# Kernel tuning notes

Hardware: AMD Instinct MI355X
Metric: run time of the kernel (lower is better)

## Reference

```python
import jax, jax.numpy as jnp
import numpy as np

B, S, D = 4, 2048, 1024
H = 16
DH = D // H  # 64
THETA = 10000.0


def setup_inputs() -> dict:
    key = jax.random.key(0)
    ks = jax.random.split(key, 7)
    scale = 1.0 / np.sqrt(D)
    return {
        "Q": jax.random.normal(ks[0], (B, S, D), dtype=jnp.float32),
        "K": jax.random.normal(ks[1], (B, S, D), dtype=jnp.float32),
        "V": jax.random.normal(ks[2], (B, S, D), dtype=jnp.float32),
        "Wq": jax.random.normal(ks[3], (D, D), dtype=jnp.float32) * scale,
        "Wk": jax.random.normal(ks[4], (D, D), dtype=jnp.float32) * scale,
        "Wv": jax.random.normal(ks[5], (D, D), dtype=jnp.float32) * scale,
        "Wo": jax.random.normal(ks[6], (D, D), dtype=jnp.float32) * scale,
    }


def _rope_tables(seq_len, d_head, theta, dtype):
    inv_freq = 1.0 / theta ** (jnp.arange(0, d_head, 2, dtype=jnp.float32) / d_head)
    ang = jnp.arange(seq_len, dtype=jnp.float32)[:, None] * inv_freq[None, :]  # [S, DH/2]
    return jnp.sin(ang).astype(dtype), jnp.cos(ang).astype(dtype)


def _apply_rope(x, sin, cos):
    # x: [B, H, S, DH]; sin/cos: [S, DH/2] broadcast over B,H
    x1 = x[..., 0::2]
    x2 = x[..., 1::2]
    x1r = x1 * cos - x2 * sin
    x2r = x1 * sin + x2 * cos
    return jnp.stack([x1r, x2r], axis=-1).reshape(x.shape)


def reference(Q, K, V, Wq, Wk, Wv, Wo):
    seq_len = Q.shape[-2]
    q = Q @ Wq.T
    k = K @ Wk.T
    v = V @ Wv.T

    def split(x):  # [B, S, D] -> [B, H, S, DH]
        return x.reshape(x.shape[0], seq_len, H, DH).transpose(0, 2, 1, 3)

    qh, kh, vh = split(q), split(k), split(v)

    sin, cos = _rope_tables(seq_len, DH, THETA, qh.dtype)
    qh = _apply_rope(qh, sin, cos)
    kh = _apply_rope(kh, sin, cos)

    # attention in fp32 (matches original cast)
    qf = qh.astype(jnp.float32)
    kf = kh.astype(jnp.float32)
    vf = vh.astype(jnp.float32)
    scale = 1.0 / np.sqrt(DH)
    scores = jnp.einsum('bhqd,bhkd->bhqk', qf, kf) * scale
    causal = jnp.tril(jnp.ones((seq_len, seq_len), dtype=bool))
    scores = jnp.where(causal, scores, -jnp.inf)
    attn = jax.nn.softmax(scores, axis=-1)
    out_h = jnp.einsum('bhqk,bhkd->bhqd', attn, vf).astype(Q.dtype)

    out = out_h.transpose(0, 2, 1, 3).reshape(Q.shape[0], seq_len, D)
    return out @ Wo.T
```

## Files before the change

kernel.cpp:

```cpp
#include <hip/hip_runtime.h>
#include <hip/hip_bf16.h>
#include <cmath>

#define B_ 4
#define S_ 2048
#define D_ 1024
#define H_ 16
#define DH_ 64

typedef __bf16 bf16_t;
typedef __bf16 bf16x8 __attribute__((ext_vector_type(8)));
typedef __bf16 bf16x4 __attribute__((ext_vector_type(4)));
typedef float f32x4 __attribute__((ext_vector_type(4)));

static __device__ __forceinline__ f32x4 mfma16(bf16x8 a, bf16x8 b, f32x4 c) {
    return __builtin_amdgcn_mfma_f32_16x16x32_bf16(a, b, c, 0, 0, 0);
}

static __device__ __forceinline__ float fast_exp2(float x) {
#if __has_builtin(__builtin_amdgcn_exp2f)
    return __builtin_amdgcn_exp2f(x);
#else
    float r; asm("v_exp_f32 %0, %1" : "=v"(r) : "v"(x)); return r;
#endif
}

static __device__ __forceinline__ void glds16(const void* g, void* l) {
    __builtin_amdgcn_global_load_lds(
        (const __attribute__((address_space(1))) unsigned int*)g,
        (__attribute__((address_space(3))) unsigned int*)l, 16, 0, 0);
}

__global__ __launch_bounds__(256)
void prep_kernel(const float* __restrict__ Wq, const float* __restrict__ Wk,
                 const float* __restrict__ Wv, const float* __restrict__ Wo,
                 bf16_t* __restrict__ Wb, float2* __restrict__ tab)
{
    int bid = blockIdx.x;
    if (bid < 256) {
        int idx = bid * 256 + threadIdx.x;
        int s = idx >> 5, i = idx & 31;
        float inv = powf(10000.f, -(2.f * i) / 64.f);
        float ang = (float)s * inv;
        tab[idx] = make_float2(sinf(ang), cosf(ang));
    } else {
        int i = (bid - 256) * 256 + threadIdx.x;
        int t = i >> 17, j = i & 131071;
        const float* src = (t == 0) ? Wq : (t == 1) ? Wk : (t == 2) ? Wv : Wo;
        const float4* s = (const float4*)(src + (size_t)j * 8);
        float4 a = s[0], b = s[1];
        bf16x8 v = { (__bf16)a.x, (__bf16)a.y, (__bf16)a.z, (__bf16)a.w,
                     (__bf16)b.x, (__bf16)b.y, (__bf16)b.z, (__bf16)b.w };
        *(bf16x8*)(Wb + (size_t)i * 8) = v;
    }
}

template<int EPI>
__global__ __launch_bounds__(256)
void proj_kernel(const float* __restrict__ X, const bf16_t* __restrict__ W,
                 bf16_t* __restrict__ dst, const float2* __restrict__ tab)
{
    __shared__ bf16x8 lA[128 * 8];
    __shared__ bf16x8 lB[128 * 8];
    const int tid = threadIdx.x;
    const int gm0 = blockIdx.x * 128;
    const int gn0 = blockIdx.y * 128;
    const int wid = tid >> 6, lane = tid & 63;
    const int lr = lane & 15, lh = lane >> 4;
    const int wm = (wid >> 1) * 64, wn = (wid & 1) * 64;

    int arow[4], aslot[4];
    const float* abase[4];
    #pragma unroll
    for (int i = 0; i < 4; ++i) {
        int slot = i * 256 + tid;
        int row = slot >> 3, s = slot & 7, c = s ^ (row & 7);
        arow[i] = row; aslot[i] = s;
        abase[i] = X + (size_t)(gm0 + row) * D_ + c * 8;
    }
    float4 av0[4], av1[4];
    #pragma unroll
    for (int i = 0; i < 4; ++i) {
        av0[i] = *(const float4*)(abase[i]);
        av1[i] = *(const float4*)(abase[i] + 4);
    }

    f32x4 acc[4][4] = {};

    #pragma unroll 1
    for (int kt = 0; kt < D_ / 64; ++kt) {
        __syncthreads();
        #pragma unroll
        for (int i = 0; i < 4; ++i) {
            int base = wid * 64 + i * 256;
            int slot = base + lane;
            int row = slot >> 3, s = slot & 7, c = s ^ (row & 7);
            glds16(W + (size_t)(gn0 + row) * D_ + kt * 64 + c * 8, &lB[base]);
        }
        #pragma unroll
        for (int i = 0; i < 4; ++i) {
            lA[arow[i] * 8 + aslot[i]] = bf16x8{
                (__bf16)av0[i].x, (__bf16)av0[i].y, (__bf16)av0[i].z, (__bf16)av0[i].w,
                (__bf16)av1[i].x, (__bf16)av1[i].y, (__bf16)av1[i].z, (__bf16)av1[i].w };
        }
        __syncthreads();
        if (kt + 1 < D_ / 64) {
            #pragma unroll
            for (int i = 0; i < 4; ++i) {
                av0[i] = *(const float4*)(abase[i] + (kt + 1) * 64);
                av1[i] = *(const float4*)(abase[i] + (kt + 1) * 64 + 4);
            }
        }
        #pragma unroll
        for (int ks = 0; ks < 2; ++ks) {
            bf16x8 af[4], bfr[4];
            int kh8 = ks * 4 + lh;
            #pragma unroll
            for (int mi = 0; mi < 4; ++mi) { int r = wm + mi * 16 + lr; af[mi]  = lA[r * 8 + (kh8 ^ (r & 7))]; }
            #pragma unroll
            for (int ni = 0; ni < 4; ++ni) { int r = wn + ni * 16 + lr; bfr[ni] = lB[r * 8 + (kh8 ^ (r & 7))]; }
            #pragma unroll
            for (int mi = 0; mi < 4; ++mi)
                #pragma unroll
                for (int ni = 0; ni < 4; ++ni)
                    acc[mi][ni] = mfma16(af[mi], bfr[ni], acc[mi][ni]);
        }
    }

    #pragma unroll
    for (int mi = 0; mi < 4; ++mi) {
        #pragma unroll
        for (int j = 0; j < 4; ++j) {
            int m = gm0 + wm + mi * 16 + lh * 4 + j;
            int b = m >> 11, s = m & (S_ - 1);
            #pragma unroll
            for (int ni = 0; ni < 4; ++ni) {
                int n = gn0 + wn + ni * 16 + lr;
                int h = n >> 6, dh = n & 63;
                float x = acc[mi][ni][j];
                if (EPI == 0) {
                    float p = __shfl_xor(x, 1);
                    float2 sc = tab[s * 32 + (dh >> 1)];
                    float r = (dh & 1) ? (p * sc.x + x * sc.y)
                                       : (x * sc.y - p * sc.x);
                    dst[(((size_t)b * H_ + h) * S_ + s) * DH_ + dh] = (bf16_t)r;
                } else {
                    dst[(((size_t)b * H_ + h) * DH_ + dh) * S_ + s] = (bf16_t)x;
                }
            }
        }
    }
}

__global__ __launch_bounds__(256, 6)
void attn_kernel(const bf16_t* __restrict__ qh, const bf16_t* __restrict__ kh,
                 const bf16_t* __restrict__ vT, bf16_t* __restrict__ O)
{
    __shared__ bf16x8 lK[64 * 8];
    __shared__ bf16x8 lV[64 * 8];
    __shared__ bf16x8 lP8[4][128];
    const int tid = threadIdx.x, wid = tid >> 6, lane = tid & 63;
    const int lr = lane & 15, lh = lane >> 4;
    const int bh = blockIdx.x & 63;
    const int t  = 31 - (blockIdx.x >> 6);
    const bf16_t* Qp = qh + (size_t)bh * S_ * DH_;
    const bf16_t* Kp = kh + (size_t)bh * S_ * DH_;
    const bf16_t* Vp = vT + (size_t)bh * DH_ * S_;
    char* lP = (char*)lP8[wid];
    const int b = bh >> 4, h = bh & 15;
    const float QSCALE = 0.125f * 1.44269504f;
    const int wq = t * 64 + wid * 16;

    bf16x8 qf[2];
    #pragma unroll
    for (int ks = 0; ks < 2; ++ks) {
        bf16x8 q8 = *(const bf16x8*)(Qp + (size_t)(wq + lr) * DH_ + ks * 32 + lh * 8);
        #pragma unroll
        for (int e = 0; e < 8; ++e) q8[e] = (__bf16)((float)q8[e] * QSCALE);
        qf[ks] = q8;
    }

    f32x4 accO[4] = {};
    float mrun = -1e30f, lrun = 0.f;
    const int nkt = t + 1;

    #pragma unroll 1
    for (int kt = 0; kt < nkt; ++kt) {
        __syncthreads();
        #pragma unroll
        for (int i = 0; i < 2; ++i) {
            int base = i * 256 + (wid << 6);
            int slot = base + lane;
            int row = slot >> 3, s = slot & 7, c = s ^ (row & 7);
            glds16(Kp + (size_t)(kt * 64 + row) * DH_ + c * 8, &lK[base]);
            glds16(Vp + (size_t)row * S_ + kt * 64 + c * 8, &lV[base]);
        }
        __syncthreads();

        f32x4 sc[4] = {};
        __builtin_amdgcn_s_setprio(1);
        #pragma unroll
        for (int ks = 0; ks < 2; ++ks) {
            int kh8 = ks * 4 + lh;
            #pragma unroll
            for (int kvi = 0; kvi < 4; ++kvi) {
                int r = kvi * 16 + lr;
                bf16x8 kf = lK[r * 8 + (kh8 ^ (r & 7))];
                sc[kvi] = mfma16(kf, qf[ks], sc[kvi]);
            }
        }
        __builtin_amdgcn_s_setprio(0);

        const int kvb = kt * 64 + 4 * lh;
        const int qg = wq + lr;
        float pv[16];
        if (kt == t) {
            #pragma unroll
            for (int kvi = 0; kvi < 4; ++kvi)
                #pragma unroll
                for (int j = 0; j < 4; ++j) {
                    float x = sc[kvi][j];
                    if ((kvb + kvi * 16 + j) > qg) x = -1e30f;
                    pv[kvi * 4 + j] = x;
                }
        } else {
            #pragma unroll
            for (int kvi = 0; kvi < 4; ++kvi)
                #pragma unroll
                for (int j = 0; j < 4; ++j) pv[kvi * 4 + j] = sc[kvi][j];
        }

        float t0 = fmaxf(fmaxf(pv[0],  pv[1]),  pv[2]);
        float t1 = fmaxf(fmaxf(pv[3],  pv[4]),  pv[5]);
        float t2 = fmaxf(fmaxf(pv[6],  pv[7]),  pv[8]);
        float t3 = fmaxf(fmaxf(pv[9],  pv[10]), pv[11]);
        float t4 = fmaxf(fmaxf(pv[12], pv[13]), pv[14]);
        float u0 = fmaxf(fmaxf(t0, t1), t2);
        float u1 = fmaxf(fmaxf(t3, t4), pv[15]);
        float mxp = fmaxf(u0, u1);

        float mnew = mrun;
        bool skip = __all(mxp <= mrun + 8.0f);
        if (!skip) {
            float mx = fmaxf(mxp, __shfl_xor(mxp, 16));
            mx = fmaxf(mx, __shfl_xor(mx, 32));
            mnew = fmaxf(mrun, mx);
            float rs = fast_exp2(mrun - mnew);
            mrun = mnew;
            lrun *= rs;
            #pragma unroll
            for (int j = 0; j < 4; ++j) {
                float rj = __shfl(rs, 4 * lh + j);
                #pragma unroll
                for (int ni = 0; ni < 4; ++ni) accO[ni][j] *= rj;
            }
        }
        #pragma unroll
        for (int i = 0; i < 16; ++i) pv[i] = fast_exp2(pv[i] - mnew);
        float s8[8], s4v[4];
        #pragma unroll
        for (int i = 0; i < 8; ++i) s8[i] = pv[i] + pv[i + 8];
        #pragma unroll
        for (int i = 0; i < 4; ++i) s4v[i] = s8[i] + s8[i + 4];
        lrun += (s4v[0] + s4v[1]) + (s4v[2] + s4v[3]);

        #pragma unroll
        for (int kvi = 0; kvi < 4; ++kvi) {
            bf16x4 hv = { (__bf16)pv[kvi * 4 + 0], (__bf16)pv[kvi * 4 + 1],
                          (__bf16)pv[kvi * 4 + 2], (__bf16)pv[kvi * 4 + 3] };
            int slot = 2 * kvi + (lh >> 1);
            *(bf16x4*)(lP + lr * 128 + ((slot ^ (lr & 7)) * 16) + (lh & 1) * 8) = hv;
        }

        __builtin_amdgcn_s_setprio(1);
        #pragma unroll
        for (int ks = 0; ks < 2; ++ks) {
            int kh8 = ks * 4 + lh;
            int slot = 4 * ks + lh;
            bf16x8 pf = *(const bf16x8*)(lP + lr * 128 + ((slot ^ (lr & 7)) * 16));
            #pragma unroll
            for (int ni = 0; ni < 4; ++ni) {
                int r = ni * 16 + lr;
                bf16x8 vf = lV[r * 8 + (kh8 ^ (r & 7))];
                accO[ni] = mfma16(pf, vf, accO[ni]);
            }
        }
        __builtin_amdgcn_s_setprio(0);
    }

    lrun += __shfl_xor(lrun, 16);
    lrun += __shfl_xor(lrun, 32);

    #pragma unroll
    for (int j = 0; j < 4; ++j) {
        int s = wq + 4 * lh + j;
        float inv = 1.f / __shfl(lrun, 4 * lh + j);
        #pragma unroll
        for (int ni = 0; ni < 4; ++ni) {
            int dh = ni * 16 + lr;
            O[((size_t)(b * S_ + s)) * D_ + h * DH_ + dh] = (bf16_t)(accO[ni][j] * inv);
        }
    }
}

__global__ __launch_bounds__(256)
void out_kernel(const bf16_t* __restrict__ A, const bf16_t* __restrict__ W,
                float* __restrict__ out)
{
    __shared__ bf16x8 lA[128 * 8];
    __shared__ bf16x8 lB[128 * 8];
    const int tid = threadIdx.x;
    const int gm0 = blockIdx.x * 128;
    const int gn0 = blockIdx.y * 128;
    const int wid = tid >> 6, lane = tid & 63;
    const int lr = lane & 15, lh = lane >> 4;
    const int wm = (wid >> 1) * 64, wn = (wid & 1) * 64;

    f32x4 acc[4][4] = {};

    for (int kt = 0; kt < D_ / 64; ++kt) {
        const int k0 = kt * 64;
        __syncthreads();
        #pragma unroll
        for (int i = 0; i < 4; ++i) {
            int base = wid * 64 + i * 256;
            int slot = base + lane;
            int row = slot >> 3, s = slot & 7, c = s ^ (row & 7);
            glds16(A + (size_t)(gm0 + row) * D_ + k0 + c * 8, &lA[base]);
            glds16(W + (size_t)(gn0 + row) * D_ + k0 + c * 8, &lB[base]);
        }
        __syncthreads();
        #pragma unroll
        for (int ks = 0; ks < 2; ++ks) {
            bf16x8 af[4], bfr[4];
            int kh = ks * 4 + lh;
            #pragma unroll
            for (int mi = 0; mi < 4; ++mi) { int r = wm + mi * 16 + lr; af[mi]  = lA[r * 8 + (kh ^ (r & 7))]; }
            #pragma unroll
            for (int ni = 0; ni < 4; ++ni) { int r = wn + ni * 16 + lr; bfr[ni] = lB[r * 8 + (kh ^ (r & 7))]; }
            #pragma unroll
            for (int mi = 0; mi < 4; ++mi)
                #pragma unroll
                for (int ni = 0; ni < 4; ++ni)
                    acc[mi][ni] = mfma16(af[mi], bfr[ni], acc[mi][ni]);
        }
    }

    #pragma unroll
    for (int mi = 0; mi < 4; ++mi)
        #pragma unroll
        for (int j = 0; j < 4; ++j) {
            int m = gm0 + wm + mi * 16 + lh * 4 + j;
            #pragma unroll
            for (int ni = 0; ni < 4; ++ni) {
                int n = gn0 + wn + ni * 16 + lr;
                out[(size_t)m * D_ + n] = acc[mi][ni][j];
            }
        }
}

extern "C" void kernel_launch(void* const* d_in, const int* in_sizes, int n_in,
                              void* d_out, int out_size, void* d_ws, size_t ws_size,
                              hipStream_t stream)
{
    const float* Q  = (const float*)d_in[0];
    const float* K  = (const float*)d_in[1];
    const float* V  = (const float*)d_in[2];
    const float* Wq = (const float*)d_in[3];
    const float* Wk = (const float*)d_in[4];
    const float* Wv = (const float*)d_in[5];
    const float* Wo = (const float*)d_in[6];
    float* out = (float*)d_out;

    char* ws = (char*)d_ws;
    const size_t MB = 1024 * 1024;
    bf16_t* qh  = (bf16_t*)(ws);
    bf16_t* khb = (bf16_t*)(ws + 16 * MB);
    bf16_t* vT  = (bf16_t*)(ws + 32 * MB);
    bf16_t* Ob  = (bf16_t*)(ws + 48 * MB);
    bf16_t* Wb  = (bf16_t*)(ws + 64 * MB);
    float2* tab = (float2*)(ws + 72 * MB);

    prep_kernel<<<2304, 256, 0, stream>>>(Wq, Wk, Wv, Wo, Wb, tab);

    dim3 g(64, 8);
    proj_kernel<0><<<g, 256, 0, stream>>>(Q, Wb + 0 * 1048576, qh, tab);
    proj_kernel<0><<<g, 256, 0, stream>>>(K, Wb + 1 * 1048576, khb, tab);
    proj_kernel<1><<<g, 256, 0, stream>>>(V, Wb + 2 * 1048576, vT, tab);

    attn_kernel<<<2048, 256, 0, stream>>>(qh, khb, vT, Ob);

    out_kernel<<<dim3(64, 8), 256, 0, stream>>>(Ob, Wb + 3 * 1048576, out);
}
```

Measured before the change: 180.2 us.

## Double-buffer LDS tiles in projection and output GEMMs to overlap loads

Both the QKV projection GEMM and the output GEMM now use two LDS buffers per operand. The next K-tile is prefetched (glds16 for W/A, register-staged fp32 converted to bf16 for X) while MFMAs run on the current tile, and only one barrier is needed per iteration instead of two. The aim is to hide global-to-LDS latency behind compute. In exchange, LDS use per block doubles, which may lower occupancy. Correctness also depends on the async glds16 writes finishing before the barrier.

```diff
diff --git a/kernel.cpp b/kernel.cpp
--- a/kernel.cpp
+++ b/kernel.cpp
@@ -60,8 +60,8 @@
 void proj_kernel(const float* __restrict__ X, const bf16_t* __restrict__ W,
                  bf16_t* __restrict__ dst, const float2* __restrict__ tab)
 {
-    __shared__ bf16x8 lA[128 * 8];
-    __shared__ bf16x8 lB[128 * 8];
+    __shared__ bf16x8 lA[2][128 * 8];
+    __shared__ bf16x8 lB[2][128 * 8];
     const int tid = threadIdx.x;
     const int gm0 = blockIdx.x * 128;
     const int gn0 = blockIdx.y * 128;
@@ -78,33 +78,42 @@
         arow[i] = row; aslot[i] = s;
         abase[i] = X + (size_t)(gm0 + row) * D_ + c * 8;
     }
+    const bf16_t* bsrc[4]; int bbase[4];
+    #pragma unroll
+    for (int i = 0; i < 4; ++i) {
+        int base = wid * 64 + i * 256;
+        int slot = base + lane;
+        int row = slot >> 3, s = slot & 7, c = s ^ (row & 7);
+        bbase[i] = base;
+        bsrc[i] = W + (size_t)(gn0 + row) * D_ + c * 8;
+    }
+
     float4 av0[4], av1[4];
     #pragma unroll
     for (int i = 0; i < 4; ++i) {
         av0[i] = *(const float4*)(abase[i]);
         av1[i] = *(const float4*)(abase[i] + 4);
     }
+    #pragma unroll
+    for (int i = 0; i < 4; ++i) glds16(bsrc[i], &lB[0][bbase[i]]);
+    #pragma unroll
+    for (int i = 0; i < 4; ++i) {
+        lA[0][arow[i] * 8 + aslot[i]] = bf16x8{
+            (__bf16)av0[i].x, (__bf16)av0[i].y, (__bf16)av0[i].z, (__bf16)av0[i].w,
+            (__bf16)av1[i].x, (__bf16)av1[i].y, (__bf16)av1[i].z, (__bf16)av1[i].w };
+    }
+    __syncthreads();
 
     f32x4 acc[4][4] = {};
+    int cur = 0;
 
     #pragma unroll 1
     for (int kt = 0; kt < D_ / 64; ++kt) {
-        __syncthreads();
-        #pragma unroll
-        for (int i = 0; i < 4; ++i) {
-            int base = wid * 64 + i * 256;
-            int slot = base + lane;
-            int row = slot >> 3, s = slot & 7, c = s ^ (row & 7);
-            glds16(W + (size_t)(gn0 + row) * D_ + kt * 64 + c * 8, &lB[base]);
-        }
-        #pragma unroll
-        for (int i = 0; i < 4; ++i) {
-            lA[arow[i] * 8 + aslot[i]] = bf16x8{
-                (__bf16)av0[i].x, (__bf16)av0[i].y, (__bf16)av0[i].z, (__bf16)av0[i].w,
-                (__bf16)av1[i].x, (__bf16)av1[i].y, (__bf16)av1[i].z, (__bf16)av1[i].w };
-        }
-        __syncthreads();
+        const int nxt = cur ^ 1;
         if (kt + 1 < D_ / 64) {
+            #pragma unroll
+            for (int i = 0; i < 4; ++i)
+                glds16(bsrc[i] + (kt + 1) * 64, &lB[nxt][bbase[i]]);
             #pragma unroll
             for (int i = 0; i < 4; ++i) {
                 av0[i] = *(const float4*)(abase[i] + (kt + 1) * 64);
@@ -116,15 +125,25 @@
             bf16x8 af[4], bfr[4];
             int kh8 = ks * 4 + lh;
             #pragma unroll
-            for (int mi = 0; mi < 4; ++mi) { int r = wm + mi * 16 + lr; af[mi]  = lA[r * 8 + (kh8 ^ (r & 7))]; }
-            #pragma unroll
-            for (int ni = 0; ni < 4; ++ni) { int r = wn + ni * 16 + lr; bfr[ni] = lB[r * 8 + (kh8 ^ (r & 7))]; }
+            for (int mi = 0; mi < 4; ++mi) { int r = wm + mi * 16 + lr; af[mi]  = lA[cur][r * 8 + (kh8 ^ (r & 7))]; }
+            #pragma unroll
+            for (int ni = 0; ni < 4; ++ni) { int r = wn + ni * 16 + lr; bfr[ni] = lB[cur][r * 8 + (kh8 ^ (r & 7))]; }
             #pragma unroll
             for (int mi = 0; mi < 4; ++mi)
                 #pragma unroll
                 for (int ni = 0; ni < 4; ++ni)
                     acc[mi][ni] = mfma16(af[mi], bfr[ni], acc[mi][ni]);
         }
+        if (kt + 1 < D_ / 64) {
+            #pragma unroll
+            for (int i = 0; i < 4; ++i) {
+                lA[nxt][arow[i] * 8 + aslot[i]] = bf16x8{
+                    (__bf16)av0[i].x, (__bf16)av0[i].y, (__bf16)av0[i].z, (__bf16)av0[i].w,
+                    (__bf16)av1[i].x, (__bf16)av1[i].y, (__bf16)av1[i].z, (__bf16)av1[i].w };
+            }
+        }
+        __syncthreads();
+        cur = nxt;
     }
 
     #pragma unroll
@@ -307,8 +326,8 @@
 void out_kernel(const bf16_t* __restrict__ A, const bf16_t* __restrict__ W,
                 float* __restrict__ out)
 {
-    __shared__ bf16x8 lA[128 * 8];
-    __shared__ bf16x8 lB[128 * 8];
+    __shared__ bf16x8 lA[2][128 * 8];
+    __shared__ bf16x8 lB[2][128 * 8];
     const int tid = threadIdx.x;
     const int gm0 = blockIdx.x * 128;
     const int gn0 = blockIdx.y * 128;
@@ -316,34 +335,53 @@
     const int lr = lane & 15, lh = lane >> 4;
     const int wm = (wid >> 1) * 64, wn = (wid & 1) * 64;
 
+    const bf16_t* asrc[4]; const bf16_t* bsrc[4]; int sbase[4];
+    #pragma unroll
+    for (int i = 0; i < 4; ++i) {
+        int base = wid * 64 + i * 256;
+        int slot = base + lane;
+        int row = slot >> 3, s = slot & 7, c = s ^ (row & 7);
+        sbase[i] = base;
+        asrc[i] = A + (size_t)(gm0 + row) * D_ + c * 8;
+        bsrc[i] = W + (size_t)(gn0 + row) * D_ + c * 8;
+    }
+
+    #pragma unroll
+    for (int i = 0; i < 4; ++i) {
+        glds16(asrc[i], &lA[0][sbase[i]]);
+        glds16(bsrc[i], &lB[0][sbase[i]]);
+    }
+    __syncthreads();
+
     f32x4 acc[4][4] = {};
-
+    int cur = 0;
+
+    #pragma unroll 1
     for (int kt = 0; kt < D_ / 64; ++kt) {
-        const int k0 = kt * 64;
-        __syncthreads();
-        #pragma unroll
-        for (int i = 0; i < 4; ++i) {
-            int base = wid * 64 + i * 256;
-            int slot = base + lane;
-            int row = slot >> 3, s = slot & 7, c = s ^ (row & 7);
-            glds16(A + (size_t)(gm0 + row) * D_ + k0 + c * 8, &lA[base]);
-            glds16(W + (size_t)(gn0 + row) * D_ + k0 + c * 8, &lB[base]);
-        }
-        __syncthreads();
+        const int nxt = cur ^ 1;
+        if (kt + 1 < D_ / 64) {
+            #pragma unroll
+            for (int i = 0; i < 4; ++i) {
+                glds16(asrc[i] + (kt + 1) * 64, &lA[nxt][sbase[i]]);
+                glds16(bsrc[i] + (kt + 1) * 64, &lB[nxt][sbase[i]]);
+            }
+        }
         #pragma unroll
         for (int ks = 0; ks < 2; ++ks) {
             bf16x8 af[4], bfr[4];
             int kh = ks * 4 + lh;
             #pragma unroll
-            for (int mi = 0; mi < 4; ++mi) { int r = wm + mi * 16 + lr; af[mi]  = lA[r * 8 + (kh ^ (r & 7))]; }
-            #pragma unroll
-            for (int ni = 0; ni < 4; ++ni) { int r = wn + ni * 16 + lr; bfr[ni] = lB[r * 8 + (kh ^ (r & 7))]; }
+            for (int mi = 0; mi < 4; ++mi) { int r = wm + mi * 16 + lr; af[mi]  = lA[cur][r * 8 + (kh ^ (r & 7))]; }
+            #pragma unroll
+            for (int ni = 0; ni < 4; ++ni) { int r = wn + ni * 16 + lr; bfr[ni] = lB[cur][r * 8 + (kh ^ (r & 7))]; }
             #pragma unroll
             for (int mi = 0; mi < 4; ++mi)
                 #pragma unroll
                 for (int ni = 0; ni < 4; ++ni)
                     acc[mi][ni] = mfma16(af[mi], bfr[ni], acc[mi][ni]);
         }
+        __syncthreads();
+        cur = nxt;
     }
 
     #pragma unroll
```

Result: faster. 175.2 us, median of 3 (-2.8%).
